# Optimization experiments

Hardware: AMD Instinct MI355X
Metric: run time of the kernel (lower is better)

## Reference

```python
import jax, jax.numpy as jnp
import numpy as np

NX, NY = 1024, 1024
N_VALUES = 64
N_CLASSES = 16
TEMPERATURE = 1.0  # forward() default
EPS = 1e-10


def setup_inputs() -> dict:
    key = jax.random.key(0)
    ks = jax.random.split(key, 5)
    x = jnp.linspace(0.0, 1.0, NX, dtype=jnp.float32)
    y = jnp.linspace(0.0, 1.0, NY, dtype=jnp.float32)
    gx, gy = jnp.meshgrid(x, y, indexing='ij')  # [NX,NY]
    return {
        'x_pos': gx.reshape(-1),                                   # [B]
        'y_pos': gy.reshape(-1),                                   # [B]
        'split_points': jax.random.uniform(ks[0], (N_VALUES,), jnp.float32) * 0.6 + 0.2,
        'split_directions_logits': jax.random.normal(ks[1], (N_VALUES,), jnp.float32),
        'class_logits': jax.random.normal(ks[2], (N_VALUES, N_CLASSES), jnp.float32),
        'child_selection_logits': jax.random.normal(ks[3], (N_VALUES, 2, N_VALUES), jnp.float32),
        'max_depth': 10,
    }


def reference(x_pos, y_pos, split_points, split_directions_logits, class_logits,
              child_selection_logits, max_depth):
    B = x_pos.shape[0]
    N = split_points.shape[0]
    t = TEMPERATURE
    dirs = jax.nn.sigmoid(split_directions_logits)                 # [N]
    # Per-point, per-node left split probability (constant over depth).
    h_left = jax.nn.sigmoid((split_points[None, :] - x_pos[:, None]) / t)  # [B,N]
    v_left = jax.nn.sigmoid((split_points[None, :] - y_pos[:, None]) / t)  # [B,N]
    left = (1.0 - dirs) * h_left + dirs * v_left                   # [B,N]
    # Node -> child routing matrices.
    L = jax.nn.softmax(child_selection_logits[:, 0, :] / t, axis=-1)  # [N,N]
    R = jax.nn.softmax(child_selection_logits[:, 1, :] / t, axis=-1)  # [N,N]

    p0 = jnp.zeros((B, N), dtype=x_pos.dtype).at[:, 0].set(1.0)

    def step(p, _):
        nxt = (p * left) @ L + (p * (1.0 - left)) @ R              # [B,N]
        nxt = nxt / jnp.clip(jnp.sum(nxt, axis=-1, keepdims=True), EPS)
        return nxt, None

    p, _ = jax.lax.scan(step, p0, None, length=int(max_depth))
    class_probs = p @ jax.nn.softmax(class_logits, axis=1)         # [B,C]
    return class_probs.reshape(NX, NY, N_CLASSES)
```

## Files before the change

### kernel.cpp

```cpp
#include <hip/hip_runtime.h>

typedef float f32x4 __attribute__((ext_vector_type(4)));
typedef _Float16 f16x8 __attribute__((ext_vector_type(8)));
typedef int i32x4 __attribute__((ext_vector_type(4)));

__device__ __forceinline__ unsigned short f2h_bits(float f) {
    _Float16 h = (_Float16)f;
    return __builtin_bit_cast(unsigned short, h);
}
__device__ __forceinline__ float sigmoidf(float x) { return 1.0f / (1.0f + expf(-x)); }

__global__ void fractal_setup_a(const float* __restrict__ csl, const float* __restrict__ cls,
                                const float* __restrict__ sp, const float* __restrict__ sdl,
                                float* __restrict__ smg, float* __restrict__ csmg,
                                float* __restrict__ tbl) {
    const int tid = threadIdx.x;
    if (blockIdx.x < 32) {
        const int w = tid >> 6;
        const int lane = tid & 63;
        const int r = blockIdx.x * 4 + w;
        const int node = r & 63;
        const int side = r >> 6;
        const float v = csl[node * 128 + side * 64 + lane];
        float mx = v;
#pragma unroll
        for (int msk = 1; msk < 64; msk <<= 1) mx = fmaxf(mx, __shfl_xor(mx, msk, 64));
        const float e = expf(v - mx);
        float sum = e;
#pragma unroll
        for (int msk = 1; msk < 64; msk <<= 1) sum += __shfl_xor(sum, msk, 64);
        smg[r * 64 + lane] = e / sum;
    } else {
        if (tid < 64) {
            const float* rowp = cls + tid * 16;
            float mx = -1e30f;
            for (int j = 0; j < 16; ++j) mx = fmaxf(mx, rowp[j]);
            float ssum = 0.f;
            for (int j = 0; j < 16; ++j) ssum += expf(rowp[j] - mx);
            const float inv = 1.0f / ssum;
            for (int j = 0; j < 16; ++j) csmg[tid * 16 + j] = expf(rowp[j] - mx) * inv;
        } else if (tid >= 128 && tid < 192) {
            tbl[tid - 128] = expf(-sp[tid - 128]);
        } else if (tid >= 192) {
            tbl[64 + tid - 192] = sigmoidf(sdl[tid - 192]);
        }
    }
}

__global__ void fractal_setup_b(const float* __restrict__ smg, const float* __restrict__ csmg,
                                unsigned short* __restrict__ frag_out,
                                float* __restrict__ row0) {
    const int e = blockIdx.x * 256 + threadIdx.x;
    if (e < 8192) {
        const int j = e & 7;
        const int l = (e >> 3) & 63;
        const int fi = e >> 9;
        const int t = fi >> 2, c = fi & 3;
        const int i = l & 15;
        const int n = 8 * (i >> 2) + (i & 3) + 4 * (t & 1) + 32 * (t >> 1);
        const int k0 = (c & 1) * 32 + (l >> 4) * 8 + j;
        float v;
        if (c < 2) v = smg[(64 + k0) * 64 + n];
        else       v = smg[k0 * 64 + n] - smg[(64 + k0) * 64 + n];
        frag_out[e] = f2h_bits(v);
    } else if (e < 9216) {
        const int e2 = e - 8192;
        const int j = e2 & 7;
        const int l = (e2 >> 3) & 63;
        const int c = e2 >> 9;
        const int n = l & 15;
        const int k = c * 32 + (l >> 4) * 8 + j;
        frag_out[8192 + e2] = f2h_bits(csmg[k * 16 + n]);
    } else if (e < 11264) {
        const int e3 = e - 9216;
        const int f = e3 >> 9;
        const int rem = e3 & 511;
        const int j = rem & 7;
        const int l = (rem >> 3) & 63;
        const int cls = l & 15;
        const int k = (f & 1) * 32 + ((l >> 4) << 3) + j;
        float acc = 0.f;
        if (f < 2) {
            for (int n = 0; n < 64; ++n)
                acc += smg[(64 + k) * 64 + n] * csmg[n * 16 + cls];
        } else {
            for (int n = 0; n < 64; ++n)
                acc += (smg[k * 64 + n] - smg[(64 + k) * 64 + n]) * csmg[n * 16 + cls];
        }
        frag_out[9216 + e3] = f2h_bits(acc);
    } else if (e < 11392) {
        const int e2 = e - 11264;
        row0[e2] = (e2 < 64) ? smg[4096 + e2]
                             : (smg[e2 - 64] - smg[4096 + (e2 - 64)]);
    }
}

__device__ __forceinline__ void fractal_step(const f16x8 (&bfr)[4][4],
                                             const f16x8& lfA0, const f16x8& lfA1,
                                             const f16x8& lfB0, const f16x8& lfB1,
                                             i32x4& puA0, i32x4& puA1,
                                             i32x4& puB0, i32x4& puB1) {
    const f16x8 pfA0 = __builtin_bit_cast(f16x8, puA0);
    const f16x8 pfA1 = __builtin_bit_cast(f16x8, puA1);
    const f16x8 pfB0 = __builtin_bit_cast(f16x8, puB0);
    const f16x8 pfB1 = __builtin_bit_cast(f16x8, puB1);
    const f16x8 aA0 = pfA0 * lfA0;
    const f16x8 aA1 = pfA1 * lfA1;
    const f16x8 aB0 = pfB0 * lfB0;
    const f16x8 aB1 = pfB1 * lfB1;
    int PA[4], QA[4], PB[4], QB[4];
#pragma unroll
    for (int t = 0; t < 4; ++t) {
        f32x4 CA = {0.f, 0.f, 0.f, 0.f};
        f32x4 CB = {0.f, 0.f, 0.f, 0.f};
        CA = __builtin_amdgcn_mfma_f32_16x16x32_f16(bfr[t][0], pfA0, CA, 0, 0, 0);
        CB = __builtin_amdgcn_mfma_f32_16x16x32_f16(bfr[t][0], pfB0, CB, 0, 0, 0);
        CA = __builtin_amdgcn_mfma_f32_16x16x32_f16(bfr[t][1], pfA1, CA, 0, 0, 0);
        CB = __builtin_amdgcn_mfma_f32_16x16x32_f16(bfr[t][1], pfB1, CB, 0, 0, 0);
        CA = __builtin_amdgcn_mfma_f32_16x16x32_f16(bfr[t][2], aA0, CA, 0, 0, 0);
        CB = __builtin_amdgcn_mfma_f32_16x16x32_f16(bfr[t][2], aB0, CB, 0, 0, 0);
        CA = __builtin_amdgcn_mfma_f32_16x16x32_f16(bfr[t][3], aA1, CA, 0, 0, 0);
        CB = __builtin_amdgcn_mfma_f32_16x16x32_f16(bfr[t][3], aB1, CB, 0, 0, 0);
        PA[t] = __builtin_bit_cast(int, __builtin_amdgcn_cvt_pkrtz(CA[0], CA[1]));
        QA[t] = __builtin_bit_cast(int, __builtin_amdgcn_cvt_pkrtz(CA[2], CA[3]));
        PB[t] = __builtin_bit_cast(int, __builtin_amdgcn_cvt_pkrtz(CB[0], CB[1]));
        QB[t] = __builtin_bit_cast(int, __builtin_amdgcn_cvt_pkrtz(CB[2], CB[3]));
    }
    puA0.x = PA[0]; puA0.y = QA[0]; puA0.z = PA[1]; puA0.w = QA[1];
    puA1.x = PA[2]; puA1.y = QA[2]; puA1.z = PA[3]; puA1.w = QA[3];
    puB0.x = PB[0]; puB0.y = QB[0]; puB0.z = PB[1]; puB0.w = QB[1];
    puB1.x = PB[2]; puB1.y = QB[2]; puB1.z = PB[3]; puB1.w = QB[3];
}

__global__ __launch_bounds__(256, 2)
void fractal_main(const float* __restrict__ x_pos, const float* __restrict__ y_pos,
                  const int* __restrict__ mdp,
                  const unsigned short* __restrict__ frags,
                  const float* __restrict__ tbl,
                  const float* __restrict__ row0,
                  const float* __restrict__ csmg,
                  float* __restrict__ out) {
    const int tid = threadIdx.x;
    const int w = tid >> 6;
    const int l = tid & 63;
    const int q = l >> 4;
    const int m = l & 15;
    const int rowbase = (blockIdx.x * 4 + w) * 32;

    const int md = mdp[0];
    if (md == 0) {
        const f32x4 cv = *(const f32x4*)(csmg + 4 * q);
        float s = cv[0] + cv[1] + cv[2] + cv[3];
        s += __shfl_xor(s, 16, 64);
        s += __shfl_xor(s, 32, 64);
        const float inv = 1.0f / fmaxf(s, 1e-10f);
        f32x4 res;
#pragma unroll
        for (int r = 0; r < 4; ++r) res[r] = cv[r] * inv;
        *(f32x4*)(out + (rowbase + m) * 16 + 4 * q) = res;
        *(f32x4*)(out + (rowbase + 16 + m) * 16 + 4 * q) = res;
        return;
    }

    const f16x8* __restrict__ fgp = (const f16x8*)frags;
    f16x8 bfr[4][4];
#pragma unroll
    for (int t = 0; t < 4; ++t)
#pragma unroll
        for (int c = 0; c < 4; ++c) bfr[t][c] = fgp[(t * 4 + c) * 64 + l];

    f32x4 tE0[2], tE1[2], tD0[2], tD1[2];
    tE0[0] = *(const f32x4*)(tbl + 8 * q);       tE0[1] = *(const f32x4*)(tbl + 8 * q + 4);
    tE1[0] = *(const f32x4*)(tbl + 32 + 8 * q);  tE1[1] = *(const f32x4*)(tbl + 32 + 8 * q + 4);
    tD0[0] = *(const f32x4*)(tbl + 64 + 8 * q);  tD0[1] = *(const f32x4*)(tbl + 64 + 8 * q + 4);
    tD1[0] = *(const f32x4*)(tbl + 96 + 8 * q);  tD1[1] = *(const f32x4*)(tbl + 96 + 8 * q + 4);

    const float xA = x_pos[rowbase + m],      yA = y_pos[rowbase + m];
    const float xB = x_pos[rowbase + 16 + m], yB = y_pos[rowbase + 16 + m];
    const float exA = __expf(xA), eyA = __expf(yA);
    const float exB = __expf(xB), eyB = __expf(yB);

    f16x8 lfA0, lfA1, lfB0, lfB1;
#pragma unroll
    for (int j = 0; j < 8; ++j) {
        const float E0 = tE0[j >> 2][j & 3];
        const float E1 = tE1[j >> 2][j & 3];
        const float d0 = tD0[j >> 2][j & 3];
        const float d1 = tD1[j >> 2][j & 3];
        {
            const float h0 = __builtin_amdgcn_rcpf(__builtin_fmaf(exA, E0, 1.0f));
            const float v0 = __builtin_amdgcn_rcpf(__builtin_fmaf(eyA, E0, 1.0f));
            const float h1 = __builtin_amdgcn_rcpf(__builtin_fmaf(exA, E1, 1.0f));
            const float v1 = __builtin_amdgcn_rcpf(__builtin_fmaf(eyA, E1, 1.0f));
            lfA0[j] = (_Float16)(h0 + d0 * (v0 - h0));
            lfA1[j] = (_Float16)(h1 + d1 * (v1 - h1));
        }
        {
            const float h0 = __builtin_amdgcn_rcpf(__builtin_fmaf(exB, E0, 1.0f));
            const float v0 = __builtin_amdgcn_rcpf(__builtin_fmaf(eyB, E0, 1.0f));
            const float h1 = __builtin_amdgcn_rcpf(__builtin_fmaf(exB, E1, 1.0f));
            const float v1 = __builtin_amdgcn_rcpf(__builtin_fmaf(eyB, E1, 1.0f));
            lfB0[j] = (_Float16)(h0 + d0 * (v0 - h0));
            lfB1[j] = (_Float16)(h1 + d1 * (v1 - h1));
        }
    }

    i32x4 puA0, puA1, puB0, puB1;
    if (md >= 2) {
        const float E00 = tbl[0];
        const float dir0 = tbl[64];
        float lA, lB;
        {
            const float h = __builtin_amdgcn_rcpf(__builtin_fmaf(exA, E00, 1.0f));
            const float v = __builtin_amdgcn_rcpf(__builtin_fmaf(eyA, E00, 1.0f));
            lA = h + dir0 * (v - h);
        }
        {
            const float h = __builtin_amdgcn_rcpf(__builtin_fmaf(exB, E00, 1.0f));
            const float v = __builtin_amdgcn_rcpf(__builtin_fmaf(eyB, E00, 1.0f));
            lB = h + dir0 * (v - h);
        }
        f32x4 rRa[2], rRb[2], rDa[2], rDb[2];
        rRa[0] = *(const f32x4*)(row0 + 8 * q);       rRa[1] = *(const f32x4*)(row0 + 8 * q + 4);
        rRb[0] = *(const f32x4*)(row0 + 32 + 8 * q);  rRb[1] = *(const f32x4*)(row0 + 32 + 8 * q + 4);
        rDa[0] = *(const f32x4*)(row0 + 64 + 8 * q);  rDa[1] = *(const f32x4*)(row0 + 64 + 8 * q + 4);
        rDb[0] = *(const f32x4*)(row0 + 96 + 8 * q);  rDb[1] = *(const f32x4*)(row0 + 96 + 8 * q + 4);
        f16x8 pA0, pA1, pB0, pB1;
#pragma unroll
        for (int j = 0; j < 8; ++j) {
            const float R0 = rRa[j >> 2][j & 3], R1 = rRb[j >> 2][j & 3];
            const float D0 = rDa[j >> 2][j & 3], D1 = rDb[j >> 2][j & 3];
            pA0[j] = (_Float16)__builtin_fmaf(lA, D0, R0);
            pA1[j] = (_Float16)__builtin_fmaf(lA, D1, R1);
            pB0[j] = (_Float16)__builtin_fmaf(lB, D0, R0);
            pB1[j] = (_Float16)__builtin_fmaf(lB, D1, R1);
        }
        puA0 = __builtin_bit_cast(i32x4, pA0);
        puA1 = __builtin_bit_cast(i32x4, pA1);
        puB0 = __builtin_bit_cast(i32x4, pB0);
        puB1 = __builtin_bit_cast(i32x4, pB1);

        if (md == 10) {
#pragma unroll
            for (int d = 0; d < 8; ++d)
                fractal_step(bfr, lfA0, lfA1, lfB0, lfB1, puA0, puA1, puB0, puB1);
        } else {
            for (int d = 0; d < md - 2; ++d)
                fractal_step(bfr, lfA0, lfA1, lfB0, lfB1, puA0, puA1, puB0, puB1);
        }
    } else {
        puA0 = (i32x4){0, 0, 0, 0}; puA1 = (i32x4){0, 0, 0, 0};
        puB0 = (i32x4){0, 0, 0, 0}; puB1 = (i32x4){0, 0, 0, 0};
        if (q == 0) { puA0.x = 0x3C00; puB0.x = 0x3C00; }
    }

    f16x8 bfin[4];
#pragma unroll
    for (int f = 0; f < 4; ++f) bfin[f] = fgp[1152 + f * 64 + l];

    {
        const f16x8 pf0 = __builtin_bit_cast(f16x8, puA0);
        const f16x8 pf1 = __builtin_bit_cast(f16x8, puA1);
        const f16x8 a0 = pf0 * lfA0;
        const f16x8 a1 = pf1 * lfA1;
        f32x4 o = {0.f, 0.f, 0.f, 0.f};
        o = __builtin_amdgcn_mfma_f32_16x16x32_f16(bfin[0], pf0, o, 0, 0, 0);
        o = __builtin_amdgcn_mfma_f32_16x16x32_f16(bfin[1], pf1, o, 0, 0, 0);
        o = __builtin_amdgcn_mfma_f32_16x16x32_f16(bfin[2], a0, o, 0, 0, 0);
        o = __builtin_amdgcn_mfma_f32_16x16x32_f16(bfin[3], a1, o, 0, 0, 0);
        float s = o[0] + o[1] + o[2] + o[3];
        s += __shfl_xor(s, 16, 64);
        s += __shfl_xor(s, 32, 64);
        const float inv = 1.0f / fmaxf(s, 1e-10f);
        f32x4 res;
#pragma unroll
        for (int r = 0; r < 4; ++r) res[r] = o[r] * inv;
        *(f32x4*)(out + (rowbase + m) * 16 + 4 * q) = res;
    }
    {
        const f16x8 pf0 = __builtin_bit_cast(f16x8, puB0);
        const f16x8 pf1 = __builtin_bit_cast(f16x8, puB1);
        const f16x8 a0 = pf0 * lfB0;
        const f16x8 a1 = pf1 * lfB1;
        f32x4 o = {0.f, 0.f, 0.f, 0.f};
        o = __builtin_amdgcn_mfma_f32_16x16x32_f16(bfin[0], pf0, o, 0, 0, 0);
        o = __builtin_amdgcn_mfma_f32_16x16x32_f16(bfin[1], pf1, o, 0, 0, 0);
        o = __builtin_amdgcn_mfma_f32_16x16x32_f16(bfin[2], a0, o, 0, 0, 0);
        o = __builtin_amdgcn_mfma_f32_16x16x32_f16(bfin[3], a1, o, 0, 0, 0);
        float s = o[0] + o[1] + o[2] + o[3];
        s += __shfl_xor(s, 16, 64);
        s += __shfl_xor(s, 32, 64);
        const float inv = 1.0f / fmaxf(s, 1e-10f);
        f32x4 res;
#pragma unroll
        for (int r = 0; r < 4; ++r) res[r] = o[r] * inv;
        *(f32x4*)(out + (rowbase + 16 + m) * 16 + 4 * q) = res;
    }
}

extern "C" void kernel_launch(void* const* d_in, const int* in_sizes, int n_in,
                              void* d_out, int out_size, void* d_ws, size_t ws_size,
                              hipStream_t stream) {
    const float* x_pos = (const float*)d_in[0];
    const float* y_pos = (const float*)d_in[1];
    const float* sp    = (const float*)d_in[2];
    const float* sdl   = (const float*)d_in[3];
    const float* cls   = (const float*)d_in[4];
    const float* csl   = (const float*)d_in[5];
    const int*   mdp   = (const int*)d_in[6];

    unsigned short* frags = (unsigned short*)d_ws;
    float* tbl  = (float*)((char*)d_ws + 22528);
    float* row0 = (float*)((char*)d_ws + 23040);
    float* smg  = (float*)((char*)d_ws + 23552);
    float* csmg = (float*)((char*)d_ws + 56320);

    fractal_setup_a<<<33, 256, 0, stream>>>(csl, cls, sp, sdl, smg, csmg, tbl);
    fractal_setup_b<<<45, 256, 0, stream>>>(smg, csmg, frags, row0);

    const int B = in_sizes[0];
    fractal_main<<<B / 128, 256, 0, stream>>>(x_pos, y_pos, mdp, frags, tbl, row0,
                                              csmg, (float*)d_out);
}
```

Before: 189.1 us.

## Process four 16-row tiles per wave to interleave independent MFMA chains

Each wave now handles 64 points (four 16-row tiles) instead of 32, so each step issues four independent MFMA accumulation chains per B fragment. This is meant to hide MFMA dependency latency and amortize the fragment and table loads over more rows, with half as many blocks launched. In exchange, register pressure roughly doubles for the state and split-probability fragments, which may cause spills under launch_bounds(256,2), and with fewer blocks the grid may not fill all CUs as well.

```diff
diff --git a/kernel.cpp b/kernel.cpp
--- a/kernel.cpp
+++ b/kernel.cpp
@@ -95,41 +95,46 @@
     }
 }
 
-__device__ __forceinline__ void fractal_step(const f16x8 (&bfr)[4][4],
-                                             const f16x8& lfA0, const f16x8& lfA1,
-                                             const f16x8& lfB0, const f16x8& lfB1,
-                                             i32x4& puA0, i32x4& puA1,
-                                             i32x4& puB0, i32x4& puB1) {
-    const f16x8 pfA0 = __builtin_bit_cast(f16x8, puA0);
-    const f16x8 pfA1 = __builtin_bit_cast(f16x8, puA1);
-    const f16x8 pfB0 = __builtin_bit_cast(f16x8, puB0);
-    const f16x8 pfB1 = __builtin_bit_cast(f16x8, puB1);
-    const f16x8 aA0 = pfA0 * lfA0;
-    const f16x8 aA1 = pfA1 * lfA1;
-    const f16x8 aB0 = pfB0 * lfB0;
-    const f16x8 aB1 = pfB1 * lfB1;
-    int PA[4], QA[4], PB[4], QB[4];
+__device__ __forceinline__ void fractal_step4(const f16x8 (&bfr)[4][4],
+                                              const f16x8 (&lf)[4][2],
+                                              i32x4 (&pu)[4][2]) {
+    f16x8 pf[4][2], a[4][2];
+#pragma unroll
+    for (int c = 0; c < 4; ++c) {
+        pf[c][0] = __builtin_bit_cast(f16x8, pu[c][0]);
+        pf[c][1] = __builtin_bit_cast(f16x8, pu[c][1]);
+        a[c][0] = pf[c][0] * lf[c][0];
+        a[c][1] = pf[c][1] * lf[c][1];
+    }
+    int P[4][4], Q[4][4];
 #pragma unroll
     for (int t = 0; t < 4; ++t) {
-        f32x4 CA = {0.f, 0.f, 0.f, 0.f};
-        f32x4 CB = {0.f, 0.f, 0.f, 0.f};
-        CA = __builtin_amdgcn_mfma_f32_16x16x32_f16(bfr[t][0], pfA0, CA, 0, 0, 0);
-        CB = __builtin_amdgcn_mfma_f32_16x16x32_f16(bfr[t][0], pfB0, CB, 0, 0, 0);
-        CA = __builtin_amdgcn_mfma_f32_16x16x32_f16(bfr[t][1], pfA1, CA, 0, 0, 0);
-        CB = __builtin_amdgcn_mfma_f32_16x16x32_f16(bfr[t][1], pfB1, CB, 0, 0, 0);
-        CA = __builtin_amdgcn_mfma_f32_16x16x32_f16(bfr[t][2], aA0, CA, 0, 0, 0);
-        CB = __builtin_amdgcn_mfma_f32_16x16x32_f16(bfr[t][2], aB0, CB, 0, 0, 0);
-        CA = __builtin_amdgcn_mfma_f32_16x16x32_f16(bfr[t][3], aA1, CA, 0, 0, 0);
-        CB = __builtin_amdgcn_mfma_f32_16x16x32_f16(bfr[t][3], aB1, CB, 0, 0, 0);
-        PA[t] = __builtin_bit_cast(int, __builtin_amdgcn_cvt_pkrtz(CA[0], CA[1]));
-        QA[t] = __builtin_bit_cast(int, __builtin_amdgcn_cvt_pkrtz(CA[2], CA[3]));
-        PB[t] = __builtin_bit_cast(int, __builtin_amdgcn_cvt_pkrtz(CB[0], CB[1]));
-        QB[t] = __builtin_bit_cast(int, __builtin_amdgcn_cvt_pkrtz(CB[2], CB[3]));
-    }
-    puA0.x = PA[0]; puA0.y = QA[0]; puA0.z = PA[1]; puA0.w = QA[1];
-    puA1.x = PA[2]; puA1.y = QA[2]; puA1.z = PA[3]; puA1.w = QA[3];
-    puB0.x = PB[0]; puB0.y = QB[0]; puB0.z = PB[1]; puB0.w = QB[1];
-    puB1.x = PB[2]; puB1.y = QB[2]; puB1.z = PB[3]; puB1.w = QB[3];
+        f32x4 C[4];
+#pragma unroll
+        for (int c = 0; c < 4; ++c) C[c] = (f32x4){0.f, 0.f, 0.f, 0.f};
+#pragma unroll
+        for (int c = 0; c < 4; ++c)
+            C[c] = __builtin_amdgcn_mfma_f32_16x16x32_f16(bfr[t][0], pf[c][0], C[c], 0, 0, 0);
+#pragma unroll
+        for (int c = 0; c < 4; ++c)
+            C[c] = __builtin_amdgcn_mfma_f32_16x16x32_f16(bfr[t][1], pf[c][1], C[c], 0, 0, 0);
+#pragma unroll
+        for (int c = 0; c < 4; ++c)
+            C[c] = __builtin_amdgcn_mfma_f32_16x16x32_f16(bfr[t][2], a[c][0], C[c], 0, 0, 0);
+#pragma unroll
+        for (int c = 0; c < 4; ++c)
+            C[c] = __builtin_amdgcn_mfma_f32_16x16x32_f16(bfr[t][3], a[c][1], C[c], 0, 0, 0);
+#pragma unroll
+        for (int c = 0; c < 4; ++c) {
+            P[c][t] = __builtin_bit_cast(int, __builtin_amdgcn_cvt_pkrtz(C[c][0], C[c][1]));
+            Q[c][t] = __builtin_bit_cast(int, __builtin_amdgcn_cvt_pkrtz(C[c][2], C[c][3]));
+        }
+    }
+#pragma unroll
+    for (int c = 0; c < 4; ++c) {
+        pu[c][0].x = P[c][0]; pu[c][0].y = Q[c][0]; pu[c][0].z = P[c][1]; pu[c][0].w = Q[c][1];
+        pu[c][1].x = P[c][2]; pu[c][1].y = Q[c][2]; pu[c][1].z = P[c][3]; pu[c][1].w = Q[c][3];
+    }
 }
 
 __global__ __launch_bounds__(256, 2)
@@ -145,7 +150,7 @@
     const int l = tid & 63;
     const int q = l >> 4;
     const int m = l & 15;
-    const int rowbase = (blockIdx.x * 4 + w) * 32;
+    const int rowbase = (blockIdx.x * 4 + w) * 64;
 
     const int md = mdp[0];
     if (md == 0) {
@@ -157,8 +162,9 @@
         f32x4 res;
 #pragma unroll
         for (int r = 0; r < 4; ++r) res[r] = cv[r] * inv;
-        *(f32x4*)(out + (rowbase + m) * 16 + 4 * q) = res;
-        *(f32x4*)(out + (rowbase + 16 + m) * 16 + 4 * q) = res;
+#pragma unroll
+        for (int c = 0; c < 4; ++c)
+            *(f32x4*)(out + (rowbase + c * 16 + m) * 16 + 4 * q) = res;
         return;
     }
 
@@ -175,94 +181,89 @@
     tD0[0] = *(const f32x4*)(tbl + 64 + 8 * q);  tD0[1] = *(const f32x4*)(tbl + 64 + 8 * q + 4);
     tD1[0] = *(const f32x4*)(tbl + 96 + 8 * q);  tD1[1] = *(const f32x4*)(tbl + 96 + 8 * q + 4);
 
-    const float xA = x_pos[rowbase + m],      yA = y_pos[rowbase + m];
-    const float xB = x_pos[rowbase + 16 + m], yB = y_pos[rowbase + 16 + m];
-    const float exA = __expf(xA), eyA = __expf(yA);
-    const float exB = __expf(xB), eyB = __expf(yB);
-
-    f16x8 lfA0, lfA1, lfB0, lfB1;
+    float ex[4], ey[4];
+#pragma unroll
+    for (int c = 0; c < 4; ++c) {
+        ex[c] = __expf(x_pos[rowbase + c * 16 + m]);
+        ey[c] = __expf(y_pos[rowbase + c * 16 + m]);
+    }
+
+    f16x8 lf[4][2];
 #pragma unroll
     for (int j = 0; j < 8; ++j) {
         const float E0 = tE0[j >> 2][j & 3];
         const float E1 = tE1[j >> 2][j & 3];
         const float d0 = tD0[j >> 2][j & 3];
         const float d1 = tD1[j >> 2][j & 3];
-        {
-            const float h0 = __builtin_amdgcn_rcpf(__builtin_fmaf(exA, E0, 1.0f));
-            const float v0 = __builtin_amdgcn_rcpf(__builtin_fmaf(eyA, E0, 1.0f));
-            const float h1 = __builtin_amdgcn_rcpf(__builtin_fmaf(exA, E1, 1.0f));
-            const float v1 = __builtin_amdgcn_rcpf(__builtin_fmaf(eyA, E1, 1.0f));
-            lfA0[j] = (_Float16)(h0 + d0 * (v0 - h0));
-            lfA1[j] = (_Float16)(h1 + d1 * (v1 - h1));
-        }
-        {
-            const float h0 = __builtin_amdgcn_rcpf(__builtin_fmaf(exB, E0, 1.0f));
-            const float v0 = __builtin_amdgcn_rcpf(__builtin_fmaf(eyB, E0, 1.0f));
-            const float h1 = __builtin_amdgcn_rcpf(__builtin_fmaf(exB, E1, 1.0f));
-            const float v1 = __builtin_amdgcn_rcpf(__builtin_fmaf(eyB, E1, 1.0f));
-            lfB0[j] = (_Float16)(h0 + d0 * (v0 - h0));
-            lfB1[j] = (_Float16)(h1 + d1 * (v1 - h1));
-        }
-    }
-
-    i32x4 puA0, puA1, puB0, puB1;
+#pragma unroll
+        for (int c = 0; c < 4; ++c) {
+            const float h0 = __builtin_amdgcn_rcpf(__builtin_fmaf(ex[c], E0, 1.0f));
+            const float v0 = __builtin_amdgcn_rcpf(__builtin_fmaf(ey[c], E0, 1.0f));
+            const float h1 = __builtin_amdgcn_rcpf(__builtin_fmaf(ex[c], E1, 1.0f));
+            const float v1 = __builtin_amdgcn_rcpf(__builtin_fmaf(ey[c], E1, 1.0f));
+            lf[c][0][j] = (_Float16)(h0 + d0 * (v0 - h0));
+            lf[c][1][j] = (_Float16)(h1 + d1 * (v1 - h1));
+        }
+    }
+
+    i32x4 pu[4][2];
     if (md >= 2) {
         const float E00 = tbl[0];
         const float dir0 = tbl[64];
-        float lA, lB;
-        {
-            const float h = __builtin_amdgcn_rcpf(__builtin_fmaf(exA, E00, 1.0f));
-            const float v = __builtin_amdgcn_rcpf(__builtin_fmaf(eyA, E00, 1.0f));
-            lA = h + dir0 * (v - h);
-        }
-        {
-            const float h = __builtin_amdgcn_rcpf(__builtin_fmaf(exB, E00, 1.0f));
-            const float v = __builtin_amdgcn_rcpf(__builtin_fmaf(eyB, E00, 1.0f));
-            lB = h + dir0 * (v - h);
+        float l0[4];
+#pragma unroll
+        for (int c = 0; c < 4; ++c) {
+            const float h = __builtin_amdgcn_rcpf(__builtin_fmaf(ex[c], E00, 1.0f));
+            const float v = __builtin_amdgcn_rcpf(__builtin_fmaf(ey[c], E00, 1.0f));
+            l0[c] = h + dir0 * (v - h);
         }
         f32x4 rRa[2], rRb[2], rDa[2], rDb[2];
         rRa[0] = *(const f32x4*)(row0 + 8 * q);       rRa[1] = *(const f32x4*)(row0 + 8 * q + 4);
         rRb[0] = *(const f32x4*)(row0 + 32 + 8 * q);  rRb[1] = *(const f32x4*)(row0 + 32 + 8 * q + 4);
         rDa[0] = *(const f32x4*)(row0 + 64 + 8 * q);  rDa[1] = *(const f32x4*)(row0 + 64 + 8 * q + 4);
         rDb[0] = *(const f32x4*)(row0 + 96 + 8 * q);  rDb[1] = *(const f32x4*)(row0 + 96 + 8 * q + 4);
-        f16x8 pA0, pA1, pB0, pB1;
+        f16x8 pt[4][2];
 #pragma unroll
         for (int j = 0; j < 8; ++j) {
             const float R0 = rRa[j >> 2][j & 3], R1 = rRb[j >> 2][j & 3];
             const float D0 = rDa[j >> 2][j & 3], D1 = rDb[j >> 2][j & 3];
-            pA0[j] = (_Float16)__builtin_fmaf(lA, D0, R0);
-            pA1[j] = (_Float16)__builtin_fmaf(lA, D1, R1);
-            pB0[j] = (_Float16)__builtin_fmaf(lB, D0, R0);
-            pB1[j] = (_Float16)__builtin_fmaf(lB, D1, R1);
-        }
-        puA0 = __builtin_bit_cast(i32x4, pA0);
-        puA1 = __builtin_bit_cast(i32x4, pA1);
-        puB0 = __builtin_bit_cast(i32x4, pB0);
-        puB1 = __builtin_bit_cast(i32x4, pB1);
+#pragma unroll
+            for (int c = 0; c < 4; ++c) {
+                pt[c][0][j] = (_Float16)__builtin_fmaf(l0[c], D0, R0);
+                pt[c][1][j] = (_Float16)__builtin_fmaf(l0[c], D1, R1);
+            }
+        }
+#pragma unroll
+        for (int c = 0; c < 4; ++c) {
+            pu[c][0] = __builtin_bit_cast(i32x4, pt[c][0]);
+            pu[c][1] = __builtin_bit_cast(i32x4, pt[c][1]);
+        }
 
         if (md == 10) {
 #pragma unroll
-            for (int d = 0; d < 8; ++d)
-                fractal_step(bfr, lfA0, lfA1, lfB0, lfB1, puA0, puA1, puB0, puB1);
+            for (int d = 0; d < 8; ++d) fractal_step4(bfr, lf, pu);
         } else {
-            for (int d = 0; d < md - 2; ++d)
-                fractal_step(bfr, lfA0, lfA1, lfB0, lfB1, puA0, puA1, puB0, puB1);
+            for (int d = 0; d < md - 2; ++d) fractal_step4(bfr, lf, pu);
         }
     } else {
-        puA0 = (i32x4){0, 0, 0, 0}; puA1 = (i32x4){0, 0, 0, 0};
-        puB0 = (i32x4){0, 0, 0, 0}; puB1 = (i32x4){0, 0, 0, 0};
-        if (q == 0) { puA0.x = 0x3C00; puB0.x = 0x3C00; }
+#pragma unroll
+        for (int c = 0; c < 4; ++c) {
+            pu[c][0] = (i32x4){0, 0, 0, 0};
+            pu[c][1] = (i32x4){0, 0, 0, 0};
+            if (q == 0) pu[c][0].x = 0x3C00;
+        }
     }
 
     f16x8 bfin[4];
 #pragma unroll
     for (int f = 0; f < 4; ++f) bfin[f] = fgp[1152 + f * 64 + l];
 
-    {
-        const f16x8 pf0 = __builtin_bit_cast(f16x8, puA0);
-        const f16x8 pf1 = __builtin_bit_cast(f16x8, puA1);
-        const f16x8 a0 = pf0 * lfA0;
-        const f16x8 a1 = pf1 * lfA1;
+#pragma unroll
+    for (int c = 0; c < 4; ++c) {
+        const f16x8 pf0 = __builtin_bit_cast(f16x8, pu[c][0]);
+        const f16x8 pf1 = __builtin_bit_cast(f16x8, pu[c][1]);
+        const f16x8 a0 = pf0 * lf[c][0];
+        const f16x8 a1 = pf1 * lf[c][1];
         f32x4 o = {0.f, 0.f, 0.f, 0.f};
         o = __builtin_amdgcn_mfma_f32_16x16x32_f16(bfin[0], pf0, o, 0, 0, 0);
         o = __builtin_amdgcn_mfma_f32_16x16x32_f16(bfin[1], pf1, o, 0, 0, 0);
@@ -275,26 +276,7 @@
         f32x4 res;
 #pragma unroll
         for (int r = 0; r < 4; ++r) res[r] = o[r] * inv;
-        *(f32x4*)(out + (rowbase + m) * 16 + 4 * q) = res;
-    }
-    {
-        const f16x8 pf0 = __builtin_bit_cast(f16x8, puB0);
-        const f16x8 pf1 = __builtin_bit_cast(f16x8, puB1);
-        const f16x8 a0 = pf0 * lfB0;
-        const f16x8 a1 = pf1 * lfB1;
-        f32x4 o = {0.f, 0.f, 0.f, 0.f};
-        o = __builtin_amdgcn_mfma_f32_16x16x32_f16(bfin[0], pf0, o, 0, 0, 0);
-        o = __builtin_amdgcn_mfma_f32_16x16x32_f16(bfin[1], pf1, o, 0, 0, 0);
-        o = __builtin_amdgcn_mfma_f32_16x16x32_f16(bfin[2], a0, o, 0, 0, 0);
-        o = __builtin_amdgcn_mfma_f32_16x16x32_f16(bfin[3], a1, o, 0, 0, 0);
-        float s = o[0] + o[1] + o[2] + o[3];
-        s += __shfl_xor(s, 16, 64);
-        s += __shfl_xor(s, 32, 64);
-        const float inv = 1.0f / fmaxf(s, 1e-10f);
-        f32x4 res;
-#pragma unroll
-        for (int r = 0; r < 4; ++r) res[r] = o[r] * inv;
-        *(f32x4*)(out + (rowbase + 16 + m) * 16 + 4 * q) = res;
+        *(f32x4*)(out + (rowbase + c * 16 + m) * 16 + 4 * q) = res;
     }
 }
 
@@ -319,6 +301,6 @@
     fractal_setup_b<<<45, 256, 0, stream>>>(smg, csmg, frags, row0);
 
     const int B = in_sizes[0];
-    fractal_main<<<B / 128, 256, 0, stream>>>(x_pos, y_pos, mdp, frags, tbl, row0,
+    fractal_main<<<B / 256, 256, 0, stream>>>(x_pos, y_pos, mdp, frags, tbl, row0,
                                               csmg, (float*)d_out);
 }
```

Measured after the change: 190.4 us. About the same (+0.7%).
